# Kernel tuning notes

Measured on AMD Instinct MI355X. Metric: run time of the kernel, lower is better.

The kernel has to match this reference:

```python
import jax, jax.numpy as jnp
import numpy as np

N, D, H, B = 8192, 1024, 100, 32  # pairs, key dim, MLP hidden, batch_size


def setup_inputs() -> dict:
    key = jax.random.key(0)
    ks = jax.random.split(key, 6)
    q = jax.random.normal(ks[0], (N, D), jnp.float32)
    x = jax.random.normal(ks[1], (N, D), jnp.float32)
    b = jax.random.randint(ks[2], (N,), 0, B, dtype=jnp.int32)
    y = jax.random.randint(ks[3], (N,), 0, 2, dtype=jnp.int32)
    # Encoder params: Linear(2D -> H), ReLU, Linear(H -> 1)
    W1 = jax.random.normal(ks[4], (2 * D, H), jnp.float32) * (1.0 / np.sqrt(2 * D))
    b1 = jnp.zeros((H,), jnp.float32)
    W2 = jax.random.normal(ks[5], (H, 1), jnp.float32) * (1.0 / np.sqrt(H))
    b2 = jnp.zeros((1,), jnp.float32)
    return {"b": b, "q": q, "x": x, "y": y, "W1": W1, "b1": b1, "W2": W2, "b2": b2}


def reference(b, q, x, y, W1, b1, W2, b2):
    # Encoder: score per (query, key) pair
    inp = jnp.concatenate([q, x], axis=1)              # (N, 2D)
    h = jax.nn.relu(inp @ W1 + b1)                     # (N, H)
    s = (h @ W2 + b2)[:, 0]                            # (N,)

    n = s.shape[0]
    r = jnp.arange(n)
    yb = y.astype(bool)
    # pair mask: same batch element, differing labels, upper triangle
    m = (b[:, None] == b[None, :]) \
        & (yb[:, None] ^ yb[None, :]) \
        & (r[:, None] < r[None, :])                    # (N, N) bool

    d = s[:, None] - s[None, :]                        # (N, N) score diffs (logits)
    z = y.astype(jnp.float32)[:, None]                 # row label broadcast as target
    # stable BCE-with-logits, masked mean (== BCEWithLogitsLoss over selected pairs)
    bce = jnp.maximum(d, 0.0) - d * z + jnp.log1p(jnp.exp(-jnp.abs(d)))
    mf = m.astype(jnp.float32)
    loss = jnp.sum(bce * mf) / jnp.sum(mf)
    return loss
```

## Files before the change

### kernel.cpp

```cpp
#include <hip/hip_runtime.h>
#include <math.h>
#include <stdint.h>

#define NN 8192
#define DD 1024
#define KT 2048
#define HH 100
#define HP 128
#define LCAP 512
#define NB 32
#define BKC 64
#define NBH 16

typedef short bf16x8 __attribute__((ext_vector_type(8)));
typedef short bf16x4 __attribute__((ext_vector_type(4)));
typedef float f32x4 __attribute__((ext_vector_type(4)));

__device__ __forceinline__ short f2bf(float f) {
    uint32_t u = __builtin_bit_cast(uint32_t, f);
    u += 0x7FFF + ((u >> 16) & 1);
    return (short)(u >> 16);
}

__global__ __launch_bounds__(256) void prep_w1p(const float* __restrict__ W1,
                                                short* __restrict__ w1p,
                                                int* __restrict__ cnt1,
                                                int* __restrict__ cnt0)
{
    __shared__ float ld[32][104];
    const int t  = threadIdx.x;
    if (blockIdx.x == 0 && t < 64) {
        if (t < 32) cnt1[t] = 0; else cnt0[t - 32] = 0;
    }
    const int k0 = blockIdx.x * 32;
    for (int i = t; i < 32 * HH; i += 256) {
        const int kk = i / HH, cc = i - kk * HH;
        ld[kk][cc] = W1[(size_t)(k0 + kk) * HH + cc];
    }
    __syncthreads();
    for (int idx = t; idx < 512; idx += 256) {
        const int tt = idx >> 6, l = idx & 63;
        const int lr = l & 15, lg = l >> 4;
        const int col = tt * 16 + lr;
        bf16x8 r;
#pragma unroll
        for (int j = 0; j < 8; ++j)
            r[j] = (col < HH) ? f2bf(ld[lg * 8 + j][col]) : (short)0;
        *(bf16x8*)(w1p + ((size_t)(blockIdx.x * 8 + tt) * 64 + l) * 8) = r;
    }
}

__global__ __launch_bounds__(512) void encoder_mfma(
    const float* __restrict__ q, const float* __restrict__ x,
    const short* __restrict__ w1p,
    const float* __restrict__ b1, const float* __restrict__ W2,
    const float* __restrict__ b2,
    const int* __restrict__ bidx, const int* __restrict__ y,
    float* __restrict__ sp, float* __restrict__ sn,
    int* __restrict__ cnt1, int* __restrict__ cnt0)
{
    __shared__ short As[2][3][16][64];
    __shared__ float fold[8][16];
    const int t    = threadIdx.x;
    const int w    = t >> 6;
    const int half = w >> 2;
    const int wc   = w & 3;
    const int l    = t & 63;
    const int lr   = l & 15;
    const int lg   = l >> 4;
    const int r0   = blockIdx.x * 16;

    const int ts    = t & 255;
    const int srow  = ts >> 4;
    const int sslot = ts & 15;
    const int wslot = sslot ^ srow;
    const float* abase = (half ? x : q) + (size_t)(r0 + srow) * DD + sslot * 4;
    auto aptr  = [&](int c) -> const float* { return abase + c * BKC; };
    auto stage = [&](int buf, const float4& v) {
        bf16x4 s;
        s[0] = f2bf(v.x); s[1] = f2bf(v.y); s[2] = f2bf(v.z); s[3] = f2bf(v.w);
        *(bf16x4*)&As[half][buf][srow][wslot * 4] = s;
    };

    const int p0 = ((2 * lg)     ^ lr) * 4;
    const int p1 = ((2 * lg + 1) ^ lr) * 4;
    const int p2 = ((2 * lg + 8) ^ lr) * 4;
    const int p3 = ((2 * lg + 9) ^ lr) * 4;

    const short* pB = w1p + (size_t)half * NBH * 8192
                    + ((size_t)(2 * wc) * 64 + l) * 8;
#define LOADB(c, x0, x1, x2, x3)                           \
    { const size_t e_ = (size_t)(c) * 8192;                \
      x0 = *(const bf16x8*)(pB + e_);                      \
      x1 = *(const bf16x8*)(pB + e_ + 4096);               \
      x2 = *(const bf16x8*)(pB + e_ + 512);                \
      x3 = *(const bf16x8*)(pB + e_ + 4096 + 512); }

    f32x4 acc0 = (f32x4)0.f, acc1 = (f32x4)0.f;
    bf16x8 bA0, bA1, bA2, bA3, bB0, bB1, bB2, bB3;

#define FRAGS_MFMA(rb, b0, b1_, b2_, b3_)                                   \
    { const short* ar = &As[half][rb][lr][0];                               \
      bf16x4 g0 = *(const bf16x4*)(ar + p0);                                \
      bf16x4 g1 = *(const bf16x4*)(ar + p1);                                \
      bf16x4 g2 = *(const bf16x4*)(ar + p2);                                \
      bf16x4 g3 = *(const bf16x4*)(ar + p3);                                \
      bf16x8 aa0 = __builtin_shufflevector(g0, g1, 0,1,2,3,4,5,6,7);        \
      bf16x8 aa1 = __builtin_shufflevector(g2, g3, 0,1,2,3,4,5,6,7);        \
      acc0 = __builtin_amdgcn_mfma_f32_16x16x32_bf16(aa0, b0,  acc0, 0,0,0);\
      acc0 = __builtin_amdgcn_mfma_f32_16x16x32_bf16(aa1, b1_, acc0, 0,0,0);\
      acc1 = __builtin_amdgcn_mfma_f32_16x16x32_bf16(aa0, b2_, acc1, 0,0,0);\
      acc1 = __builtin_amdgcn_mfma_f32_16x16x32_bf16(aa1, b3_, acc1, 0,0,0); }

    float4 t0 = *(const float4*)aptr(0);
    float4 t1 = *(const float4*)aptr(1);
    float4 rE = *(const float4*)aptr(2);
    float4 rO = *(const float4*)aptr(3);
    LOADB(0, bA0, bA1, bA2, bA3);
    stage(0, t0);
    stage(1, t1);
    __syncthreads();

    int rb = 0;
#pragma unroll 1
    for (int c = 0; c < NBH; c += 2) {
        { const int cn = c + 1 < NBH ? c + 1 : NBH - 1; LOADB(cn, bB0, bB1, bB2, bB3); }
        FRAGS_MFMA(rb, bA0, bA1, bA2, bA3);
        __syncthreads();
        { int wb = rb - 1; if (wb < 0) wb = 2;
          stage(wb, rE);
          rE = *(const float4*)aptr(c + 4 < NBH ? c + 4 : NBH - 1); }
        rb = (rb == 2) ? 0 : rb + 1;
        { const int cn = c + 2 < NBH ? c + 2 : NBH - 1; LOADB(cn, bA0, bA1, bA2, bA3); }
        FRAGS_MFMA(rb, bB0, bB1, bB2, bB3);
        __syncthreads();
        { int wb = rb - 1; if (wb < 0) wb = 2;
          stage(wb, rO);
          rO = *(const float4*)aptr(c + 5 < NBH ? c + 5 : NBH - 1); }
        rb = (rb == 2) ? 0 : rb + 1;
    }

    __shared__ float hsum[16][HP + 4];
    if (half == 0) {
#pragma unroll
        for (int r = 0; r < 4; ++r) {
            hsum[lg * 4 + r][wc * 32 + lr]      = acc0[r];
            hsum[lg * 4 + r][wc * 32 + lr + 16] = acc1[r];
        }
    }
    __syncthreads();
    if (half == 1) {
#pragma unroll
        for (int r = 0; r < 4; ++r) {
            hsum[lg * 4 + r][wc * 32 + lr]      += acc0[r];
            hsum[lg * 4 + r][wc * 32 + lr + 16] += acc1[r];
        }
    }
    __syncthreads();
    if (half == 0) {
        const int c0 = wc * 32 + lr;
        const int c1 = c0 + 16;
        const float bb0 = (c0 < HH) ? b1[c0] : 0.f;
        const float ww0 = (c0 < HH) ? W2[c0] : 0.f;
        const float bb1 = (c1 < HH) ? b1[c1] : 0.f;
        const float ww1 = (c1 < HH) ? W2[c1] : 0.f;
#pragma unroll
        for (int r = 0; r < 4; ++r) {
            const int row = lg * 4 + r;
            float v = fmaf(fmaxf(hsum[row][c0] + bb0, 0.f), ww0,
                           fmaxf(hsum[row][c1] + bb1, 0.f) * ww1);
            v += __shfl_xor(v, 1);
            v += __shfl_xor(v, 2);
            v += __shfl_xor(v, 4);
            v += __shfl_xor(v, 8);
            if (lr == 0) fold[wc][row] = v;
        }
    }
    __syncthreads();
    if (t < 16) {
        const float sv = fold[0][t] + fold[1][t] + fold[2][t] + fold[3][t] + b2[0];
        const int i = r0 + t;
        const int g = bidx[i];
        if (y[i]) {
            int idx = atomicAdd(&cnt1[g], 1);
            if (idx < LCAP) sp[g * LCAP + idx] = sv;
        } else {
            int idx = atomicAdd(&cnt0[g], 1);
            if (idx < LCAP) sn[g * LCAP + idx] = sv;
        }
    }
#undef LOADB
#undef FRAGS_MFMA
}

__global__ __launch_bounds__(256) void pairsum_kernel(
    const float* __restrict__ sp, const float* __restrict__ sn,
    const int* __restrict__ cnt1, const int* __restrict__ cnt0,
    float* __restrict__ partial)
{
    __shared__ float lsn[LCAP];
    __shared__ float lsp[64];
    __shared__ float wsum[4];
    const int g  = blockIdx.x >> 3;
    const int sl = blockIdx.x & 7;
    const int t  = threadIdx.x;
    const int n1 = min(cnt1[g], LCAP);
    const int n0 = min(cnt0[g], LCAP);
    for (int j = t; j < n0; j += 256) lsn[j] = sn[g * LCAP + j];
    const int np = (n1 > sl) ? ((n1 - sl + 7) >> 3) : 0;
    for (int j = t; j < np; j += 256) lsp[j] = sp[g * LCAP + sl + j * 8];
    __syncthreads();
    float acc = 0.f;
    const int total = np * n0;
    for (int u = t; u < total; u += 256) {
        const int ip = u / n0;
        const int j  = u - ip * n0;
        const float d  = lsn[j] - lsp[ip];
        const float ad = fabsf(d);
        const float z  = __builtin_exp2f(-ad * 1.44269504f);
        acc += fmaxf(d, 0.f) + __builtin_log2f(1.f + z) * 0.69314718f;
    }
#pragma unroll
    for (int off = 32; off > 0; off >>= 1) acc += __shfl_xor(acc, off, 64);
    const int wid = t >> 6, lane = t & 63;
    if (lane == 0) wsum[wid] = acc;
    __syncthreads();
    if (t == 0) partial[blockIdx.x] = wsum[0] + wsum[1] + wsum[2] + wsum[3];
}

__global__ __launch_bounds__(256) void finalize_kernel(
    const float* __restrict__ partial,
    const int* __restrict__ cnt1, const int* __restrict__ cnt0,
    float* __restrict__ out)
{
    __shared__ float ws_[4], wc_[4];
    const int t = threadIdx.x;
    float sv = partial[t];
    float cv = 0.f;
    if (t < NB) cv = (float)min(cnt1[t], LCAP) * (float)min(cnt0[t], LCAP);
#pragma unroll
    for (int off = 32; off > 0; off >>= 1) {
        sv += __shfl_xor(sv, off, 64);
        cv += __shfl_xor(cv, off, 64);
    }
    const int wid = t >> 6, lane = t & 63;
    if (lane == 0) { ws_[wid] = sv; wc_[wid] = cv; }
    __syncthreads();
    if (t == 0)
        out[0] = (ws_[0] + ws_[1] + ws_[2] + ws_[3]) /
                 (wc_[0] + wc_[1] + wc_[2] + wc_[3]);
}

extern "C" void kernel_launch(void* const* d_in, const int* in_sizes, int n_in,
                              void* d_out, int out_size, void* d_ws, size_t ws_size,
                              hipStream_t stream)
{
    const int*   b  = (const int*)d_in[0];
    const float* q  = (const float*)d_in[1];
    const float* x  = (const float*)d_in[2];
    const int*   y  = (const int*)d_in[3];
    const float* W1 = (const float*)d_in[4];
    const float* b1 = (const float*)d_in[5];
    const float* W2 = (const float*)d_in[6];
    const float* b2 = (const float*)d_in[7];
    float* out = (float*)d_out;

    char* base = (char*)d_ws;
    short* w1p     = (short*)base;
    float* sp      = (float*)(base + 524288);
    float* sn      = (float*)(base + 524288 + 65536);
    int*   cnt1    = (int*)(base + 524288 + 131072);
    int*   cnt0    = cnt1 + NB;
    float* partial = (float*)(base + 524288 + 131072 + 256);

    prep_w1p<<<KT / 32, 256, 0, stream>>>(W1, w1p, cnt1, cnt0);
    encoder_mfma<<<NN / 16, 512, 0, stream>>>(q, x, w1p, b1, W2, b2,
                                              b, y, sp, sn, cnt1, cnt0);
    pairsum_kernel<<<NB * 8, 256, 0, stream>>>(sp, sn, cnt1, cnt0, partial);
    finalize_kernel<<<1, 256, 0, stream>>>(partial, cnt1, cnt0, out);
}
```

Before: 49.70 us.

## Stage full A tile into LDS upfront and drop per-chunk barriers in encoder

Replaces the triple-buffered streaming of A chunks, which needed a barrier per chunk, with one bulk load. The whole 16x1024 bf16 row tile of each half is read from global memory with batched float4 loads, converted and written to LDS, followed by a single barrier. The MFMA loop then reads only from LDS and keeps the software-pipelined W1 register loads, removing the per-iteration __syncthreads. The cost is a larger LDS footprint (64KB for As) and a longer prologue with no overlap between global A loads and MFMA, which may reduce occupancy.

```diff
diff --git a/kernel.cpp b/kernel.cpp
--- a/kernel.cpp
+++ b/kernel.cpp
@@ -9,8 +9,7 @@
 #define HP 128
 #define LCAP 512
 #define NB 32
-#define BKC 64
-#define NBH 16
+#define NCH 16
 
 typedef short bf16x8 __attribute__((ext_vector_type(8)));
 typedef short bf16x4 __attribute__((ext_vector_type(4)));
@@ -59,8 +58,9 @@
     float* __restrict__ sp, float* __restrict__ sn,
     int* __restrict__ cnt1, int* __restrict__ cnt0)
 {
-    __shared__ short As[2][3][16][64];
-    __shared__ float fold[8][16];
+    __shared__ short As[2][16][NCH][64];
+    __shared__ float hsum[16][HP + 4];
+    __shared__ float fold[4][16];
     const int t    = threadIdx.x;
     const int w    = t >> 6;
     const int half = w >> 2;
@@ -73,21 +73,34 @@
     const int ts    = t & 255;
     const int srow  = ts >> 4;
     const int sslot = ts & 15;
-    const int wslot = sslot ^ srow;
+    const int wslot = (sslot ^ srow) * 4;
     const float* abase = (half ? x : q) + (size_t)(r0 + srow) * DD + sslot * 4;
-    auto aptr  = [&](int c) -> const float* { return abase + c * BKC; };
-    auto stage = [&](int buf, const float4& v) {
+    auto cvt4 = [&](const float4& v) {
         bf16x4 s;
         s[0] = f2bf(v.x); s[1] = f2bf(v.y); s[2] = f2bf(v.z); s[3] = f2bf(v.w);
-        *(bf16x4*)&As[half][buf][srow][wslot * 4] = s;
+        return s;
     };
+    {
+        float4 g[8];
+#pragma unroll
+        for (int p = 0; p < 8; ++p) g[p] = *(const float4*)(abase + p * 64);
+#pragma unroll
+        for (int p = 0; p < 8; ++p)
+            *(bf16x4*)&As[half][srow][p][wslot] = cvt4(g[p]);
+#pragma unroll
+        for (int p = 0; p < 8; ++p) g[p] = *(const float4*)(abase + (p + 8) * 64);
+#pragma unroll
+        for (int p = 0; p < 8; ++p)
+            *(bf16x4*)&As[half][srow][p + 8][wslot] = cvt4(g[p]);
+    }
+    __syncthreads();
 
     const int p0 = ((2 * lg)     ^ lr) * 4;
     const int p1 = ((2 * lg + 1) ^ lr) * 4;
     const int p2 = ((2 * lg + 8) ^ lr) * 4;
     const int p3 = ((2 * lg + 9) ^ lr) * 4;
 
-    const short* pB = w1p + (size_t)half * NBH * 8192
+    const short* pB = w1p + (size_t)half * NCH * 8192
                     + ((size_t)(2 * wc) * 64 + l) * 8;
 #define LOADB(c, x0, x1, x2, x3)                           \
     { const size_t e_ = (size_t)(c) * 8192;                \
@@ -99,8 +112,8 @@
     f32x4 acc0 = (f32x4)0.f, acc1 = (f32x4)0.f;
     bf16x8 bA0, bA1, bA2, bA3, bB0, bB1, bB2, bB3;
 
-#define FRAGS_MFMA(rb, b0, b1_, b2_, b3_)                                   \
-    { const short* ar = &As[half][rb][lr][0];                               \
+#define FRAGS_MFMA(c, b0, b1_, b2_, b3_)                                    \
+    { const short* ar = &As[half][lr][c][0];                                \
       bf16x4 g0 = *(const bf16x4*)(ar + p0);                                \
       bf16x4 g1 = *(const bf16x4*)(ar + p1);                                \
       bf16x4 g2 = *(const bf16x4*)(ar + p2);                                \
@@ -112,35 +125,15 @@
       acc1 = __builtin_amdgcn_mfma_f32_16x16x32_bf16(aa0, b2_, acc1, 0,0,0);\
       acc1 = __builtin_amdgcn_mfma_f32_16x16x32_bf16(aa1, b3_, acc1, 0,0,0); }
 
-    float4 t0 = *(const float4*)aptr(0);
-    float4 t1 = *(const float4*)aptr(1);
-    float4 rE = *(const float4*)aptr(2);
-    float4 rO = *(const float4*)aptr(3);
     LOADB(0, bA0, bA1, bA2, bA3);
-    stage(0, t0);
-    stage(1, t1);
-    __syncthreads();
-
-    int rb = 0;
-#pragma unroll 1
-    for (int c = 0; c < NBH; c += 2) {
-        { const int cn = c + 1 < NBH ? c + 1 : NBH - 1; LOADB(cn, bB0, bB1, bB2, bB3); }
-        FRAGS_MFMA(rb, bA0, bA1, bA2, bA3);
-        __syncthreads();
-        { int wb = rb - 1; if (wb < 0) wb = 2;
-          stage(wb, rE);
-          rE = *(const float4*)aptr(c + 4 < NBH ? c + 4 : NBH - 1); }
-        rb = (rb == 2) ? 0 : rb + 1;
-        { const int cn = c + 2 < NBH ? c + 2 : NBH - 1; LOADB(cn, bA0, bA1, bA2, bA3); }
-        FRAGS_MFMA(rb, bB0, bB1, bB2, bB3);
-        __syncthreads();
-        { int wb = rb - 1; if (wb < 0) wb = 2;
-          stage(wb, rO);
-          rO = *(const float4*)aptr(c + 5 < NBH ? c + 5 : NBH - 1); }
-        rb = (rb == 2) ? 0 : rb + 1;
-    }
-
-    __shared__ float hsum[16][HP + 4];
+#pragma unroll 2
+    for (int c = 0; c < NCH; c += 2) {
+        LOADB(c + 1, bB0, bB1, bB2, bB3);
+        FRAGS_MFMA(c, bA0, bA1, bA2, bA3);
+        { const int cn = (c + 2 < NCH) ? c + 2 : 0; LOADB(cn, bA0, bA1, bA2, bA3); }
+        FRAGS_MFMA(c + 1, bB0, bB1, bB2, bB3);
+    }
+
     if (half == 0) {
 #pragma unroll
         for (int r = 0; r < 4; ++r) {
```

Measured after the change: 51.74 us. +4.1%, slower.
